# Kernel optimization log

Hardware: AMD Instinct MI355X
Metric: run time of the kernel (lower is better)

The kernel has to match this reference:

```python
import jax, jax.numpy as jnp
import numpy as np

B, N = 2, 512
D_NODE, D_EDGE, D_HID, H = 128, 64, 128, 8
DH = D_HID // H  # per-head dim = 16
SCALE = 1.0 / (D_HID ** 0.5)  # note: scale uses full d_hid as in source


def setup_inputs() -> dict:
    key = jax.random.key(0)
    k1, k2, k3, k4 = jax.random.split(key, 4)
    node_features = jax.random.normal(k1, (B, N, D_NODE), dtype=jnp.float32)
    edge_features = jax.random.normal(k2, (B, N, N, D_EDGE), dtype=jnp.float32)
    mask = jnp.ones((B, N, N), dtype=bool)
    # Linear weights (stored as (in, out); math identical to torch x @ W.T)
    W_node = jax.random.normal(k3, (D_NODE, 3 * D_HID), dtype=jnp.float32) / np.sqrt(D_NODE)
    W_edge = jax.random.normal(k4, (D_EDGE, 3 * D_HID), dtype=jnp.float32) / np.sqrt(D_EDGE)
    return {"node_features": node_features, "edge_features": edge_features,
            "mask": mask, "W_node": W_node, "W_edge": W_edge}


def _split_heads_node(x):
    # (b, n, h*c) -> (b, h, n, c)
    b, n, hc = x.shape
    return x.reshape(b, n, H, hc // H).transpose(0, 2, 1, 3)


def _split_heads_edge(x):
    # (b, n, m, h*c) -> (b, h, n, m, c)
    b, n, m, hc = x.shape
    return x.reshape(b, n, m, H, hc // H).transpose(0, 3, 1, 2, 4)


def reference(node_features, edge_features, mask, W_node, W_edge):
    # node qkv: (b, n, 3*d_hid) -> (b, h, n, 3*dh) -> chunk
    qkv_n = _split_heads_node(node_features @ W_node)
    q_node, k_node, v_node = jnp.split(qkv_n, 3, axis=-1)  # each (b,h,n,dh)
    # edge qkv: (b, n, n, 3*d_hid) -> (b, h, n, n, 3*dh) -> chunk
    qkv_e = _split_heads_edge(edge_features @ W_edge)
    q_edge, k_edge, v_edge = jnp.split(qkv_e, 3, axis=-1)  # each (b,h,n,n,dh)

    q = q_node[:, :, :, None, :] + q_edge   # (b,h,i,j,dh)
    k = k_node[:, :, None, :, :] + k_edge   # (b,h,i,j,dh)
    v = v_node[:, :, None, :, :] + v_edge   # (b,h,i,j,dh)

    dots = SCALE * jnp.einsum('bhijd,bhijd->bhij', q, k)
    attn = jax.nn.softmax(dots, axis=-1)
    out = jnp.einsum('bhij,bhijd->bhid', attn, v)  # (b,h,n,dh)
    # (b,h,n,dh) -> (b,n,h*dh)
    b, h, n, dh = out.shape
    return out.transpose(0, 2, 1, 3).reshape(b, n, h * dh)
```

## Files before the change

### kernel.cpp

```cpp
#include <hip/hip_runtime.h>

#define NN 512
#define OC 384
#define S2F 0.12751694f

typedef __attribute__((ext_vector_type(8))) short short8;
typedef __attribute__((ext_vector_type(4))) float f32x4;

__device__ __forceinline__ unsigned short f2bf(float x) {
    unsigned u = __builtin_bit_cast(unsigned, x);
    u = (u + 0x7fffu + ((u >> 16) & 1u)) >> 16;
    return (unsigned short)u;
}

__global__ __launch_bounds__(256) void prep0_kernel(
    const float* __restrict__ Wn, const float* __restrict__ We,
    const float* __restrict__ node,
    unsigned short* __restrict__ WtN, unsigned short* __restrict__ WtE,
    unsigned short* __restrict__ nodeBf)
{
    int idx = blockIdx.x * 256 + threadIdx.x;
    if (idx < 24576) {
        int o = idx >> 6, k = idx & 63;
        WtE[idx] = f2bf(We[k * OC + o]);
    } else if (idx < 24576 + 49152) {
        int id = idx - 24576;
        int o = id >> 7, k = id & 127;
        WtN[id] = f2bf(Wn[k * OC + o]);
    } else {
        int id = idx - 73728;
        nodeBf[id] = f2bf(node[id]);
    }
}

__global__ __launch_bounds__(256) void prep1_kernel(
    const unsigned short* __restrict__ nodeBf,
    const unsigned short* __restrict__ WtN,
    float* __restrict__ qnF,
    float* __restrict__ nodeKV)
{
    const int t = threadIdx.x;
    const int w = t >> 6;
    const int lane = t & 63;
    const int lj = lane & 15;
    const int quad = lane >> 4;
    const int nbase = blockIdx.x * 32;

    short8 bfr[2][4];
#pragma unroll
    for (int nt = 0; nt < 2; ++nt)
#pragma unroll
        for (int ks = 0; ks < 4; ++ks)
            bfr[nt][ks] = *reinterpret_cast<const short8*>(
                nodeBf + (size_t)(nbase + nt * 16 + lj) * 128 + ks * 32 + quad * 8);

#pragma unroll
    for (int m = 0; m < 6; ++m) {
        int ot = (6 * w + m) * 16;
        short8 afr[4];
#pragma unroll
        for (int ks = 0; ks < 4; ++ks)
            afr[ks] = *reinterpret_cast<const short8*>(
                WtN + (size_t)(ot + lj) * 128 + ks * 32 + quad * 8);
#pragma unroll
        for (int nt = 0; nt < 2; ++nt) {
            f32x4 acc = {0.f, 0.f, 0.f, 0.f};
#pragma unroll
            for (int ks = 0; ks < 4; ++ks)
                acc = __builtin_amdgcn_mfma_f32_16x16x32_bf16(afr[ks], bfr[nt][ks], acc, 0, 0, 0);
            int n = nbase + nt * 16 + lj;
            int bb = n >> 9, ii = n & 511;
#pragma unroll
            for (int r = 0; r < 4; ++r) {
                int o = ot + quad * 4 + r;
                int h = o / 48, rem = o - h * 48;
                size_t base = (size_t)(bb * 8 + h) * NN + ii;
                if (rem < 16) {
                    qnF[base * 16 + rem] = acc[r];
                } else {
                    int d = (rem - 16) & 15;
                    int isv = (rem >= 32) ? 4 : 0;
                    nodeKV[base * 32 + (d >> 2) * 8 + isv + (d & 3)] = acc[r];
                }
            }
        }
    }
}

__global__ __launch_bounds__(512, 4) void rt_attn_main(
    const float* __restrict__ edge,
    const float* __restrict__ qnF,
    const float* __restrict__ nodeKV,
    const unsigned short* __restrict__ WtE,
    float* __restrict__ out)
{
    __shared__ unsigned short sE[2][64 * 72];
    const int bi = blockIdx.x;
    const int b = bi >> 9;
    const int i = bi & 511;
    const int t = threadIdx.x;
    const int h = t >> 6;
    const int lane = t & 63;
    const int lj = lane & 15;
    const int quad = lane >> 4;

    const int sj0 = t >> 4;
    const int sj1 = sj0 + 32;
    const int sc = (t & 15) * 4;

    short8 afr[3][2];
#pragma unroll
    for (int T = 0; T < 3; ++T)
#pragma unroll
        for (int sec = 0; sec < 2; ++sec)
            afr[T][sec] = *reinterpret_cast<const short8*>(
                WtE + (size_t)(h * 48 + T * 16 + lj) * 64 + sec * 32 + quad * 8);

    const f32x4 qn = *reinterpret_cast<const f32x4*>(
        qnF + ((size_t)(b * 8 + h) * NN + i) * 16 + quad * 4);

    float l = 0.f;
    float oa[4] = {0.f, 0.f, 0.f, 0.f};

    const float* eBase = edge + (size_t)bi * NN * 64;
    const float* kvBase = nodeKV + (size_t)(b * 8 + h) * NN * 32;
    f32x4 pf0, pf1;

    pf0 = *reinterpret_cast<const f32x4*>(eBase + (size_t)sj0 * 64 + sc);
    pf1 = *reinterpret_cast<const f32x4*>(eBase + (size_t)sj1 * 64 + sc);
    {
        ushort4 u0, u1;
        u0.x = f2bf(pf0[0]); u0.y = f2bf(pf0[1]); u0.z = f2bf(pf0[2]); u0.w = f2bf(pf0[3]);
        u1.x = f2bf(pf1[0]); u1.y = f2bf(pf1[1]); u1.z = f2bf(pf1[2]); u1.w = f2bf(pf1[3]);
        *reinterpret_cast<ushort4*>(&sE[0][sj0 * 72 + sc]) = u0;
        *reinterpret_cast<ushort4*>(&sE[0][sj1 * 72 + sc]) = u1;
    }
    __syncthreads();

    for (int tt = 0; tt < 8; ++tt) {
        const int cur = tt & 1;
        if (tt < 7) {
            const float* nb = eBase + (size_t)(tt + 1) * 4096;
            pf0 = *reinterpret_cast<const f32x4*>(nb + (size_t)sj0 * 64 + sc);
            pf1 = *reinterpret_cast<const f32x4*>(nb + (size_t)sj1 * 64 + sc);
        }
#pragma unroll
        for (int jn = 0; jn < 4; ++jn) {
            const int jrow = jn * 16 + lj;
            const int j = tt * 64 + jrow;
            const float* kvp = kvBase + (size_t)j * 32 + quad * 8;
            f32x4 fk = *reinterpret_cast<const f32x4*>(kvp);
            f32x4 fv = *reinterpret_cast<const f32x4*>(kvp + 4);
            f32x4 fq = qn;
            short8 b0 = *reinterpret_cast<const short8*>(&sE[cur][jrow * 72 + quad * 8]);
            short8 b1 = *reinterpret_cast<const short8*>(&sE[cur][jrow * 72 + 32 + quad * 8]);
            fq = __builtin_amdgcn_mfma_f32_16x16x32_bf16(afr[0][0], b0, fq, 0, 0, 0);
            fq = __builtin_amdgcn_mfma_f32_16x16x32_bf16(afr[0][1], b1, fq, 0, 0, 0);
            fk = __builtin_amdgcn_mfma_f32_16x16x32_bf16(afr[1][0], b0, fk, 0, 0, 0);
            fk = __builtin_amdgcn_mfma_f32_16x16x32_bf16(afr[1][1], b1, fk, 0, 0, 0);
            fv = __builtin_amdgcn_mfma_f32_16x16x32_bf16(afr[2][0], b0, fv, 0, 0, 0);
            fv = __builtin_amdgcn_mfma_f32_16x16x32_bf16(afr[2][1], b1, fv, 0, 0, 0);
            float dp = fq[0] * fk[0];
            dp = fmaf(fq[1], fk[1], dp);
            dp = fmaf(fq[2], fk[2], dp);
            dp = fmaf(fq[3], fk[3], dp);
            dp += __shfl_xor(dp, 16);
            dp += __shfl_xor(dp, 32);
            float wg = exp2f(dp * S2F);
            l += wg;
#pragma unroll
            for (int r = 0; r < 4; ++r) oa[r] = fmaf(wg, fv[r], oa[r]);
        }
        if (tt < 7) {
            ushort4 u0, u1;
            u0.x = f2bf(pf0[0]); u0.y = f2bf(pf0[1]); u0.z = f2bf(pf0[2]); u0.w = f2bf(pf0[3]);
            u1.x = f2bf(pf1[0]); u1.y = f2bf(pf1[1]); u1.z = f2bf(pf1[2]); u1.w = f2bf(pf1[3]);
            *reinterpret_cast<ushort4*>(&sE[cur ^ 1][sj0 * 72 + sc]) = u0;
            *reinterpret_cast<ushort4*>(&sE[cur ^ 1][sj1 * 72 + sc]) = u1;
            __syncthreads();
        }
    }

#pragma unroll
    for (int off = 1; off <= 8; off <<= 1) {
        l += __shfl_xor(l, off);
#pragma unroll
        for (int r = 0; r < 4; ++r) oa[r] += __shfl_xor(oa[r], off);
    }
    if (lj == 0) {
        float inv = 1.0f / l;
        f32x4 o4;
#pragma unroll
        for (int r = 0; r < 4; ++r) o4[r] = oa[r] * inv;
        *reinterpret_cast<f32x4*>(out + (size_t)bi * 128 + h * 16 + quad * 4) = o4;
    }
}

extern "C" void kernel_launch(void* const* d_in, const int* in_sizes, int n_in,
                              void* d_out, int out_size, void* d_ws, size_t ws_size,
                              hipStream_t stream) {
    const float* node = (const float*)d_in[0];
    const float* edge = (const float*)d_in[1];
    const float* Wn = (const float*)d_in[3];
    const float* We = (const float*)d_in[4];
    float* out = (float*)d_out;

    char* ws = (char*)d_ws;
    float* qnF = (float*)ws;
    float* nodeKV = (float*)(ws + 524288);
    unsigned short* WtE = (unsigned short*)(ws + 1572864);
    unsigned short* WtN = (unsigned short*)(ws + 1622016);
    unsigned short* nodeBf = (unsigned short*)(ws + 1720320);

    prep0_kernel<<<800, 256, 0, stream>>>(Wn, We, node, WtN, WtE, nodeBf);
    prep1_kernel<<<32, 256, 0, stream>>>(nodeBf, WtN, qnF, nodeKV);
    rt_attn_main<<<2 * NN, 512, 0, stream>>>(edge, qnF, nodeKV, WtE, out);
}
```

Baseline: 248.1 us.

## Split attention over key chunks into partial blocks with a combine kernel

```diff
diff --git a/kernel.cpp b/kernel.cpp
--- a/kernel.cpp
+++ b/kernel.cpp
@@ -2,6 +2,7 @@
 
 #define NN 512
 #define OC 384
+#define JC 4
 #define S2F 0.12751694f
 
 typedef __attribute__((ext_vector_type(8))) short short8;
@@ -87,17 +88,21 @@
     }
 }
 
-__global__ __launch_bounds__(512, 4) void rt_attn_main(
+__global__ __launch_bounds__(512, 4) void rt_attn_part(
     const float* __restrict__ edge,
     const float* __restrict__ qnF,
     const float* __restrict__ nodeKV,
     const unsigned short* __restrict__ WtE,
-    float* __restrict__ out)
+    float* __restrict__ partO,
+    float* __restrict__ partL)
 {
     __shared__ unsigned short sE[2][64 * 72];
-    const int bi = blockIdx.x;
+    const int blk = blockIdx.x;
+    const int jc = blk >> 10;
+    const int bi = blk & 1023;
     const int b = bi >> 9;
     const int i = bi & 511;
+    const int jbase = jc * (NN / JC);
     const int t = threadIdx.x;
     const int h = t >> 6;
     const int lane = t & 63;
@@ -108,6 +113,12 @@
     const int sj1 = sj0 + 32;
     const int sc = (t & 15) * 4;
 
+    const float* eBase = edge + ((size_t)bi * NN + jbase) * 64;
+    f32x4 pf0, pf1;
+
+    pf0 = *reinterpret_cast<const f32x4*>(eBase + (size_t)sj0 * 64 + sc);
+    pf1 = *reinterpret_cast<const f32x4*>(eBase + (size_t)sj1 * 64 + sc);
+
     short8 afr[3][2];
 #pragma unroll
     for (int T = 0; T < 3; ++T)
@@ -121,13 +132,8 @@
 
     float l = 0.f;
     float oa[4] = {0.f, 0.f, 0.f, 0.f};
-
-    const float* eBase = edge + (size_t)bi * NN * 64;
     const float* kvBase = nodeKV + (size_t)(b * 8 + h) * NN * 32;
-    f32x4 pf0, pf1;
-
-    pf0 = *reinterpret_cast<const f32x4*>(eBase + (size_t)sj0 * 64 + sc);
-    pf1 = *reinterpret_cast<const f32x4*>(eBase + (size_t)sj1 * 64 + sc);
+
     {
         ushort4 u0, u1;
         u0.x = f2bf(pf0[0]); u0.y = f2bf(pf0[1]); u0.z = f2bf(pf0[2]); u0.w = f2bf(pf0[3]);
@@ -137,17 +143,17 @@
     }
     __syncthreads();
 
-    for (int tt = 0; tt < 8; ++tt) {
-        const int cur = tt & 1;
-        if (tt < 7) {
-            const float* nb = eBase + (size_t)(tt + 1) * 4096;
+    for (int tt = 0; tt < 2; ++tt) {
+        const int cur = tt;
+        if (tt == 0) {
+            const float* nb = eBase + 4096;
             pf0 = *reinterpret_cast<const f32x4*>(nb + (size_t)sj0 * 64 + sc);
             pf1 = *reinterpret_cast<const f32x4*>(nb + (size_t)sj1 * 64 + sc);
         }
 #pragma unroll
         for (int jn = 0; jn < 4; ++jn) {
             const int jrow = jn * 16 + lj;
-            const int j = tt * 64 + jrow;
+            const int j = jbase + tt * 64 + jrow;
             const float* kvp = kvBase + (size_t)j * 32 + quad * 8;
             f32x4 fk = *reinterpret_cast<const f32x4*>(kvp);
             f32x4 fv = *reinterpret_cast<const f32x4*>(kvp + 4);
@@ -171,12 +177,12 @@
 #pragma unroll
             for (int r = 0; r < 4; ++r) oa[r] = fmaf(wg, fv[r], oa[r]);
         }
-        if (tt < 7) {
+        if (tt == 0) {
             ushort4 u0, u1;
             u0.x = f2bf(pf0[0]); u0.y = f2bf(pf0[1]); u0.z = f2bf(pf0[2]); u0.w = f2bf(pf0[3]);
             u1.x = f2bf(pf1[0]); u1.y = f2bf(pf1[1]); u1.z = f2bf(pf1[2]); u1.w = f2bf(pf1[3]);
-            *reinterpret_cast<ushort4*>(&sE[cur ^ 1][sj0 * 72 + sc]) = u0;
-            *reinterpret_cast<ushort4*>(&sE[cur ^ 1][sj1 * 72 + sc]) = u1;
+            *reinterpret_cast<ushort4*>(&sE[1][sj0 * 72 + sc]) = u0;
+            *reinterpret_cast<ushort4*>(&sE[1][sj1 * 72 + sc]) = u1;
             __syncthreads();
         }
     }
@@ -187,13 +193,39 @@
 #pragma unroll
         for (int r = 0; r < 4; ++r) oa[r] += __shfl_xor(oa[r], off);
     }
+    const size_t bih = (size_t)bi * 8 + h;
     if (lj == 0) {
-        float inv = 1.0f / l;
         f32x4 o4;
 #pragma unroll
-        for (int r = 0; r < 4; ++r) o4[r] = oa[r] * inv;
-        *reinterpret_cast<f32x4*>(out + (size_t)bi * 128 + h * 16 + quad * 4) = o4;
-    }
+        for (int r = 0; r < 4; ++r) o4[r] = oa[r];
+        *reinterpret_cast<f32x4*>(partO + ((size_t)jc * 8192 + bih) * 16 + quad * 4) = o4;
+        if (quad == 0) partL[(size_t)jc * 8192 + bih] = l;
+    }
+}
+
+__global__ __launch_bounds__(256) void combine_kernel(
+    const float* __restrict__ partO,
+    const float* __restrict__ partL,
+    float* __restrict__ out)
+{
+    int tid = blockIdx.x * 256 + threadIdx.x;
+    int bih = tid >> 2;
+    int d4 = (tid & 3) << 2;
+    float l = 0.f;
+    f32x4 s = {0.f, 0.f, 0.f, 0.f};
+#pragma unroll
+    for (int jc = 0; jc < JC; ++jc) {
+        l += partL[(size_t)jc * 8192 + bih];
+        f32x4 p = *reinterpret_cast<const f32x4*>(
+            partO + ((size_t)jc * 8192 + bih) * 16 + d4);
+#pragma unroll
+        for (int r = 0; r < 4; ++r) s[r] += p[r];
+    }
+    float inv = 1.0f / l;
+    f32x4 o4;
+#pragma unroll
+    for (int r = 0; r < 4; ++r) o4[r] = s[r] * inv;
+    *reinterpret_cast<f32x4*>(out + (size_t)bih * 16 + d4) = o4;
 }
 
 extern "C" void kernel_launch(void* const* d_in, const int* in_sizes, int n_in,
@@ -211,8 +243,11 @@
     unsigned short* WtE = (unsigned short*)(ws + 1572864);
     unsigned short* WtN = (unsigned short*)(ws + 1622016);
     unsigned short* nodeBf = (unsigned short*)(ws + 1720320);
+    float* partO = (float*)(ws + 1982464);
+    float* partL = (float*)(ws + 4079616);
 
     prep0_kernel<<<800, 256, 0, stream>>>(Wn, We, node, WtN, WtE, nodeBf);
     prep1_kernel<<<32, 256, 0, stream>>>(nodeBf, WtN, qnF, nodeKV);
-    rt_attn_main<<<2 * NN, 512, 0, stream>>>(edge, qnF, nodeKV, WtE, out);
-}
+    rt_attn_part<<<JC * 1024, 512, 0, stream>>>(edge, qnF, nodeKV, WtE, partO, partL);
+    combine_kernel<<<128, 256, 0, stream>>>(partO, partL, out);
+}
```

Result: slower. 263.3 us (+6.1%).

## Load edge tiles directly into registers, dropping shared-memory staging and barriers

Applied to the files above, without the earlier changes.

```diff
diff --git a/kernel.cpp b/kernel.cpp
--- a/kernel.cpp
+++ b/kernel.cpp
@@ -1,4 +1,5 @@
 #include <hip/hip_runtime.h>
+#include <hip/hip_bf16.h>
 
 #define NN 512
 #define OC 384
@@ -11,6 +12,16 @@
     unsigned u = __builtin_bit_cast(unsigned, x);
     u = (u + 0x7fffu + ((u >> 16) & 1u)) >> 16;
     return (unsigned short)u;
+}
+
+__device__ __forceinline__ short8 cvt8(f32x4 a, f32x4 b) {
+    union { short8 s; unsigned u[4]; } r;
+    union { __hip_bfloat162 h; unsigned u; } c;
+    c.h = __float22bfloat162_rn(make_float2(a[0], a[1])); r.u[0] = c.u;
+    c.h = __float22bfloat162_rn(make_float2(a[2], a[3])); r.u[1] = c.u;
+    c.h = __float22bfloat162_rn(make_float2(b[0], b[1])); r.u[2] = c.u;
+    c.h = __float22bfloat162_rn(make_float2(b[2], b[3])); r.u[3] = c.u;
+    return r.s;
 }
 
 __global__ __launch_bounds__(256) void prep0_kernel(
@@ -87,14 +98,13 @@
     }
 }
 
-__global__ __launch_bounds__(512, 4) void rt_attn_main(
+__global__ __launch_bounds__(512) void rt_attn_main(
     const float* __restrict__ edge,
     const float* __restrict__ qnF,
     const float* __restrict__ nodeKV,
     const unsigned short* __restrict__ WtE,
     float* __restrict__ out)
 {
-    __shared__ unsigned short sE[2][64 * 72];
     const int bi = blockIdx.x;
     const int b = bi >> 9;
     const int i = bi & 511;
@@ -104,9 +114,8 @@
     const int lj = lane & 15;
     const int quad = lane >> 4;
 
-    const int sj0 = t >> 4;
-    const int sj1 = sj0 + 32;
-    const int sc = (t & 15) * 4;
+    const float* eP = edge + (size_t)bi * NN * 64 + lj * 64 + quad * 8;
+    const float* kvP = nodeKV + ((size_t)(b * 8 + h) * NN + lj) * 32 + quad * 8;
 
     short8 afr[3][2];
 #pragma unroll
@@ -122,64 +131,49 @@
     float l = 0.f;
     float oa[4] = {0.f, 0.f, 0.f, 0.f};
 
-    const float* eBase = edge + (size_t)bi * NN * 64;
-    const float* kvBase = nodeKV + (size_t)(b * 8 + h) * NN * 32;
-    f32x4 pf0, pf1;
-
-    pf0 = *reinterpret_cast<const f32x4*>(eBase + (size_t)sj0 * 64 + sc);
-    pf1 = *reinterpret_cast<const f32x4*>(eBase + (size_t)sj1 * 64 + sc);
-    {
-        ushort4 u0, u1;
-        u0.x = f2bf(pf0[0]); u0.y = f2bf(pf0[1]); u0.z = f2bf(pf0[2]); u0.w = f2bf(pf0[3]);
-        u1.x = f2bf(pf1[0]); u1.y = f2bf(pf1[1]); u1.z = f2bf(pf1[2]); u1.w = f2bf(pf1[3]);
-        *reinterpret_cast<ushort4*>(&sE[0][sj0 * 72 + sc]) = u0;
-        *reinterpret_cast<ushort4*>(&sE[0][sj1 * 72 + sc]) = u1;
-    }
-    __syncthreads();
-
-    for (int tt = 0; tt < 8; ++tt) {
-        const int cur = tt & 1;
-        if (tt < 7) {
-            const float* nb = eBase + (size_t)(tt + 1) * 4096;
-            pf0 = *reinterpret_cast<const f32x4*>(nb + (size_t)sj0 * 64 + sc);
-            pf1 = *reinterpret_cast<const f32x4*>(nb + (size_t)sj1 * 64 + sc);
-        }
-#pragma unroll
-        for (int jn = 0; jn < 4; ++jn) {
-            const int jrow = jn * 16 + lj;
-            const int j = tt * 64 + jrow;
-            const float* kvp = kvBase + (size_t)j * 32 + quad * 8;
-            f32x4 fk = *reinterpret_cast<const f32x4*>(kvp);
-            f32x4 fv = *reinterpret_cast<const f32x4*>(kvp + 4);
-            f32x4 fq = qn;
-            short8 b0 = *reinterpret_cast<const short8*>(&sE[cur][jrow * 72 + quad * 8]);
-            short8 b1 = *reinterpret_cast<const short8*>(&sE[cur][jrow * 72 + 32 + quad * 8]);
-            fq = __builtin_amdgcn_mfma_f32_16x16x32_bf16(afr[0][0], b0, fq, 0, 0, 0);
-            fq = __builtin_amdgcn_mfma_f32_16x16x32_bf16(afr[0][1], b1, fq, 0, 0, 0);
-            fk = __builtin_amdgcn_mfma_f32_16x16x32_bf16(afr[1][0], b0, fk, 0, 0, 0);
-            fk = __builtin_amdgcn_mfma_f32_16x16x32_bf16(afr[1][1], b1, fk, 0, 0, 0);
-            fv = __builtin_amdgcn_mfma_f32_16x16x32_bf16(afr[2][0], b0, fv, 0, 0, 0);
-            fv = __builtin_amdgcn_mfma_f32_16x16x32_bf16(afr[2][1], b1, fv, 0, 0, 0);
-            float dp = fq[0] * fk[0];
-            dp = fmaf(fq[1], fk[1], dp);
-            dp = fmaf(fq[2], fk[2], dp);
-            dp = fmaf(fq[3], fk[3], dp);
-            dp += __shfl_xor(dp, 16);
-            dp += __shfl_xor(dp, 32);
-            float wg = exp2f(dp * S2F);
-            l += wg;
-#pragma unroll
-            for (int r = 0; r < 4; ++r) oa[r] = fmaf(wg, fv[r], oa[r]);
-        }
-        if (tt < 7) {
-            ushort4 u0, u1;
-            u0.x = f2bf(pf0[0]); u0.y = f2bf(pf0[1]); u0.z = f2bf(pf0[2]); u0.w = f2bf(pf0[3]);
-            u1.x = f2bf(pf1[0]); u1.y = f2bf(pf1[1]); u1.z = f2bf(pf1[2]); u1.w = f2bf(pf1[3]);
-            *reinterpret_cast<ushort4*>(&sE[cur ^ 1][sj0 * 72 + sc]) = u0;
-            *reinterpret_cast<ushort4*>(&sE[cur ^ 1][sj1 * 72 + sc]) = u1;
-            __syncthreads();
-        }
-    }
+    f32x4 eA0[2], eA1[2], eB0[2], eB1[2], kv0[2], kv1[2];
+#define ISSUE(jn, s)                                                          \
+    do {                                                                      \
+        const float* ep_ = eP + (size_t)(jn) * 1024;                          \
+        eA0[s] = *reinterpret_cast<const f32x4*>(ep_);                        \
+        eA1[s] = *reinterpret_cast<const f32x4*>(ep_ + 4);                    \
+        eB0[s] = *reinterpret_cast<const f32x4*>(ep_ + 32);                   \
+        eB1[s] = *reinterpret_cast<const f32x4*>(ep_ + 36);                   \
+        const float* kp_ = kvP + (size_t)(jn) * 512;                          \
+        kv0[s] = *reinterpret_cast<const f32x4*>(kp_);                        \
+        kv1[s] = *reinterpret_cast<const f32x4*>(kp_ + 4);                    \
+    } while (0)
+
+    ISSUE(0, 0);
+    ISSUE(1, 1);
+
+#pragma unroll 4
+    for (int jn = 0; jn < 32; ++jn) {
+        const int s = jn & 1;
+        f32x4 a0 = eA0[s], a1 = eA1[s], c0 = eB0[s], c1 = eB1[s];
+        f32x4 fk = kv0[s], fv = kv1[s];
+        if (jn < 30) ISSUE(jn + 2, s);
+        short8 B0 = cvt8(a0, a1);
+        short8 B1 = cvt8(c0, c1);
+        f32x4 fq = qn;
+        fq = __builtin_amdgcn_mfma_f32_16x16x32_bf16(afr[0][0], B0, fq, 0, 0, 0);
+        fq = __builtin_amdgcn_mfma_f32_16x16x32_bf16(afr[0][1], B1, fq, 0, 0, 0);
+        fk = __builtin_amdgcn_mfma_f32_16x16x32_bf16(afr[1][0], B0, fk, 0, 0, 0);
+        fk = __builtin_amdgcn_mfma_f32_16x16x32_bf16(afr[1][1], B1, fk, 0, 0, 0);
+        fv = __builtin_amdgcn_mfma_f32_16x16x32_bf16(afr[2][0], B0, fv, 0, 0, 0);
+        fv = __builtin_amdgcn_mfma_f32_16x16x32_bf16(afr[2][1], B1, fv, 0, 0, 0);
+        float dp = fq[0] * fk[0];
+        dp = fmaf(fq[1], fk[1], dp);
+        dp = fmaf(fq[2], fk[2], dp);
+        dp = fmaf(fq[3], fk[3], dp);
+        dp += __shfl_xor(dp, 16);
+        dp += __shfl_xor(dp, 32);
+        float wg = exp2f(dp * S2F);
+        l += wg;
+#pragma unroll
+        for (int r = 0; r < 4; ++r) oa[r] = fmaf(wg, fv[r], oa[r]);
+    }
+#undef ISSUE
 
 #pragma unroll
     for (int off = 1; off <= 8; off <<= 1) {
```

After: 339.8 us. 36.9% more time.
